# Optimization experiments

Measured on AMD Instinct MI355X. Metric: run time of the kernel, lower is better.

The kernel has to match this reference:

```python
import jax, jax.numpy as jnp
import numpy as np

B, T, HID, H = 4, 2048, 768, 12
D = HID // H  # head_dim = 64


def setup_inputs() -> dict:
    key = jax.random.key(0)
    ks = jax.random.split(key, 8)
    s = 0.02  # keep logits in a sane range
    return {
        "hidden_states": jax.random.normal(ks[0], (B, T, HID), dtype=jnp.float32),
        "attention_mask": jax.random.normal(ks[1], (B, 1, 1, T), dtype=jnp.float32),
        "Wq": jax.random.normal(ks[2], (HID, HID), dtype=jnp.float32) * s,
        "bq": jax.random.normal(ks[3], (HID,), dtype=jnp.float32) * s,
        "Wk": jax.random.normal(ks[4], (HID, HID), dtype=jnp.float32) * s,
        "bk": jax.random.normal(ks[5], (HID,), dtype=jnp.float32) * s,
        "Wv": jax.random.normal(ks[6], (HID, HID), dtype=jnp.float32) * s,
        "bv": jax.random.normal(ks[7], (HID,), dtype=jnp.float32) * s,
    }


def _split_heads(x):
    # [B, T, HID] -> [B, H, T, D]
    b, t, _ = x.shape
    return x.reshape(b, t, H, D).transpose(0, 2, 1, 3)


def reference(hidden_states, attention_mask, Wq, bq, Wk, bk, Wv, bv):
    # nn.Linear: y = x @ W^T + b
    q = _split_heads(hidden_states @ Wq.T + bq)  # [B,H,T,D]
    k = _split_heads(hidden_states @ Wk.T + bk)
    v = _split_heads(hidden_states @ Wv.T + bv)

    scores = jnp.einsum("bhqd,bhkd->bhqk", q, k) / jnp.sqrt(jnp.float32(D))
    causal = jnp.tril(jnp.ones((T, T), dtype=bool))[None, None]  # [1,1,T,T]
    neg_inf = jnp.finfo(scores.dtype).min
    scores = jnp.where(causal, scores, neg_inf)
    # attention_mask here is a float additive mask (randn: min<0, max>1 branch)
    scores = scores + attention_mask

    probs = jax.nn.softmax(scores, axis=-1)  # [B,H,T,T]
    ctx = jnp.einsum("bhqk,bhkd->bhqd", probs, v)  # [B,H,T,D]
    return ctx.transpose(0, 2, 1, 3).reshape(B, T, HID)
```

## Files before the change

### kernel.cpp

```cpp
#include <hip/hip_runtime.h>
#include <hip/hip_bf16.h>
#include <stdint.h>

typedef __attribute__((ext_vector_type(8))) short short8x;
typedef __attribute__((ext_vector_type(4))) float float4x;
typedef __attribute__((ext_vector_type(2))) unsigned int uint2x;

#define B_SZ 4
#define T_SEQ 2048
#define HID_SZ 768
#define NH 12
#define HD 64
#define LDP 72
#define QBLK 64
#define NT 32

__device__ __forceinline__ unsigned short f2b(float f) {
    union { float f; unsigned int u; } v; v.f = f;
    unsigned int u = v.u;
    u += 0x7fffu + ((u >> 16) & 1u);
    return (unsigned short)(u >> 16);
}

__device__ __forceinline__ unsigned int pkbf(float a, float b) {
    __hip_bfloat162 p = __float22bfloat162_rn(make_float2(a, b));
    return *(unsigned int*)&p;
}

__global__ __launch_bounds__(256) void qkv_gemm(
    const float* __restrict__ X,
    const float* __restrict__ Wq, const float* __restrict__ bq,
    const float* __restrict__ Wk, const float* __restrict__ bk,
    const float* __restrict__ Wv, const float* __restrict__ bv,
    unsigned short* __restrict__ Yq, unsigned short* __restrict__ Yk,
    unsigned short* __restrict__ Yv)
{
    const int z = blockIdx.z;
    const float* W    = (z == 0) ? Wq : (z == 1) ? Wk : Wv;
    const float* bias = (z == 0) ? bq : (z == 1) ? bk : bv;
    unsigned short* Y = (z == 0) ? Yq : (z == 1) ? Yk : Yv;

    __shared__ unsigned short As[128 * LDP];
    __shared__ unsigned short Bs[128 * LDP];
    const int tid  = threadIdx.x;
    const int lane = tid & 63;
    const int w    = tid >> 6;
    const int bm = blockIdx.x, bn = blockIdx.y;
    const int wm = (w >> 1) * 64, wn = (w & 1) * 64;
    const int lr = lane & 15;
    const int hi = lane >> 4;

    float4x acc[4][4];
#pragma unroll
    for (int i = 0; i < 4; ++i)
#pragma unroll
        for (int j = 0; j < 4; ++j) acc[i][j] = (float4x)0.0f;

    for (int k0 = 0; k0 < HID_SZ; k0 += 64) {
        __syncthreads();
#pragma unroll
        for (int i = 0; i < 8; ++i) {
            int f4 = tid + i * 256;
            int row = f4 >> 4, c4 = f4 & 15;
            float4 va = *(const float4*)(X + (size_t)(bm * 128 + row) * HID_SZ + k0 + c4 * 4);
            uint2x ua; ua.x = pkbf(va.x, va.y); ua.y = pkbf(va.z, va.w);
            *(uint2x*)&As[row * LDP + c4 * 4] = ua;
            float4 vb = *(const float4*)(W + (size_t)(bn * 128 + row) * HID_SZ + k0 + c4 * 4);
            uint2x ub; ub.x = pkbf(vb.x, vb.y); ub.y = pkbf(vb.z, vb.w);
            *(uint2x*)&Bs[row * LDP + c4 * 4] = ub;
        }
        __syncthreads();

        short8x a[4][2], bf[4][2];
#pragma unroll
        for (int rf = 0; rf < 4; ++rf)
#pragma unroll
            for (int ks = 0; ks < 2; ++ks)
                a[rf][ks] = *(const short8x*)&As[(wm + rf * 16 + lr) * LDP + ks * 32 + hi * 8];
#pragma unroll
        for (int cf = 0; cf < 4; ++cf)
#pragma unroll
            for (int ks = 0; ks < 2; ++ks)
                bf[cf][ks] = *(const short8x*)&Bs[(wn + cf * 16 + lr) * LDP + ks * 32 + hi * 8];
        __builtin_amdgcn_s_setprio(1);
#pragma unroll
        for (int rf = 0; rf < 4; ++rf)
#pragma unroll
            for (int cf = 0; cf < 4; ++cf)
#pragma unroll
                for (int ks = 0; ks < 2; ++ks)
                    acc[rf][cf] = __builtin_amdgcn_mfma_f32_16x16x32_bf16(
                        a[rf][ks], bf[cf][ks], acc[rf][cf], 0, 0, 0);
        __builtin_amdgcn_s_setprio(0);
    }

#pragma unroll
    for (int rf = 0; rf < 4; ++rf)
#pragma unroll
        for (int cf = 0; cf < 4; ++cf) {
            int n = bn * 128 + wn + cf * 16 + lr;
            float bv = bias[n];
            int h = n >> 6, d = n & 63;
#pragma unroll
            for (int reg = 0; reg < 4; ++reg) {
                int m = bm * 128 + wm + rf * 16 + hi * 4 + reg;
                int b = m >> 11, t = m & 2047;
                Y[(((size_t)b * NH + h) * T_SEQ + t) * HD + d] = f2b(acc[rf][cf][reg] + bv);
            }
        }
}

__global__ __launch_bounds__(256) void attn(
    const unsigned short* __restrict__ Q, const unsigned short* __restrict__ K,
    const unsigned short* __restrict__ V, const float* __restrict__ mask,
    float* __restrict__ out)
{
    __shared__ unsigned short Vt[2][HD * LDP];
    __shared__ unsigned short Ps[4][16 * LDP];
    __shared__ float Ms[T_SEQ];

    const int tid = threadIdx.x, lane = tid & 63, w = tid >> 6;
    const int lr = lane & 15, hi = lane >> 4;
    const int bh = blockIdx.x;
    const int jj = NT - 1 - blockIdx.y;
    const int b = bh / NH, h = bh % NH;
    const size_t base = (size_t)bh * T_SEQ * HD;
    const int q0 = jj * QBLK;

    {
        int t8 = tid * 8;
        *(float4*)&Ms[t8]     = *(const float4*)&mask[b * T_SEQ + t8];
        *(float4*)&Ms[t8 + 4] = *(const float4*)&mask[b * T_SEQ + t8 + 4];
    }

    const int c8 = tid & 7;
    const int r0 = tid >> 3;
    const int r1 = r0 + 32;
    const int pr0 = r0 ^ (c8 << 3);
    const int pr1 = r1 ^ (c8 << 3);

    short8x qa[2];
#pragma unroll
    for (int ks = 0; ks < 2; ++ks)
        qa[ks] = *(const short8x*)(Q + base + (size_t)(q0 + w * 16 + lr) * HD + ks * 32 + hi * 8);

    float4x o[4];
    float mrun = -3.0e38f, lrun = 0.0f;
#pragma unroll
    for (int j = 0; j < 4; ++j) o[j] = (float4x)0.0f;

    {
        short8x v0 = *(const short8x*)(V + base + (size_t)r0 * HD + c8 * 8);
        short8x v1 = *(const short8x*)(V + base + (size_t)r1 * HD + c8 * 8);
#pragma unroll
        for (int j = 0; j < 8; ++j) {
            Vt[0][(c8 * 8 + j) * LDP + pr0] = (unsigned short)v0[j];
            Vt[0][(c8 * 8 + j) * LDP + pr1] = (unsigned short)v1[j];
        }
    }
    __syncthreads();

    int cur = 0;
    int kv = 0;
    short8x kb0[4][2], kb1[4][2];
#pragma unroll
    for (int c = 0; c < 4; ++c)
#pragma unroll
        for (int ks = 0; ks < 2; ++ks)
            kb0[c][ks] = *(const short8x*)(K + base + (size_t)(c * 16 + lr) * HD + ks * 32 + hi * 8);

    auto body = [&](short8x (&kb)[4][2], short8x (&kbn)[4][2]) -> bool {
        const bool pf = (kv < jj);
        short8x nv0, nv1;
        if (pf) {
#pragma unroll
            for (int c = 0; c < 4; ++c)
#pragma unroll
                for (int ks = 0; ks < 2; ++ks)
                    kbn[c][ks] = *(const short8x*)(K + base + (size_t)((kv + 1) * 64 + c * 16 + lr) * HD + ks * 32 + hi * 8);
            nv0 = *(const short8x*)(V + base + (size_t)((kv + 1) * 64 + r0) * HD + c8 * 8);
            nv1 = *(const short8x*)(V + base + (size_t)((kv + 1) * 64 + r1) * HD + c8 * 8);
        }

        float4x s[4];
        __builtin_amdgcn_s_setprio(1);
#pragma unroll
        for (int c = 0; c < 4; ++c) {
            s[c] = (float4x)0.0f;
#pragma unroll
            for (int ks = 0; ks < 2; ++ks)
                s[c] = __builtin_amdgcn_mfma_f32_16x16x32_bf16(
                    kb[c][ks], qa[ks], s[c], 0, 0, 0);
        }
        __builtin_amdgcn_s_setprio(0);

        const bool diag = (kv == jj);
        const int qloc = w * 16 + lr;
#pragma unroll
        for (int c = 0; c < 4; ++c) {
            float4 mv = *(const float4*)&Ms[kv * 64 + c * 16 + hi * 4];
#pragma unroll
            for (int reg = 0; reg < 4; ++reg) {
                float x = s[c][reg] * 0.125f + ((const float*)&mv)[reg];
                if (diag) {
                    int kloc = c * 16 + hi * 4 + reg;
                    if (kloc > qloc) x = -1.0e30f;
                }
                s[c][reg] = x;
            }
        }

        float tm = -3.0e38f;
#pragma unroll
        for (int c = 0; c < 4; ++c)
#pragma unroll
            for (int reg = 0; reg < 4; ++reg) tm = fmaxf(tm, s[c][reg]);
        tm = fmaxf(tm, __shfl_xor(tm, 16, 64));
        tm = fmaxf(tm, __shfl_xor(tm, 32, 64));
        float mn = fmaxf(mrun, tm);
        float corr = __expf(mrun - mn);
        mrun = mn;
        float ps = 0.0f;
#pragma unroll
        for (int c = 0; c < 4; ++c)
#pragma unroll
            for (int reg = 0; reg < 4; ++reg) {
                float p = __expf(s[c][reg] - mn);
                s[c][reg] = p;
                ps += p;
            }
        ps += __shfl_xor(ps, 16, 64);
        ps += __shfl_xor(ps, 32, 64);
        lrun = lrun * corr + ps;
#pragma unroll
        for (int cf = 0; cf < 4; ++cf) o[cf] *= corr;

#pragma unroll
        for (int c = 0; c < 4; ++c) {
            uint2x pk;
            pk.x = pkbf(s[c][0], s[c][1]);
            pk.y = pkbf(s[c][2], s[c][3]);
            *(uint2x*)&Ps[w][lr * LDP + c * 16 + hi * 4] = pk;
        }

        short8x pa[2], vb[4][2];
#pragma unroll
        for (int ks = 0; ks < 2; ++ks)
            pa[ks] = *(const short8x*)&Ps[w][lr * LDP + ks * 32 + hi * 8];
#pragma unroll
        for (int cf = 0; cf < 4; ++cf)
#pragma unroll
            for (int ks = 0; ks < 2; ++ks) {
                int d = cf * 16 + lr;
                int pcb = (ks * 32 + hi * 8) ^ (((d >> 3) & 7) << 3);
                vb[cf][ks] = *(const short8x*)&Vt[cur][d * LDP + pcb];
            }
        __builtin_amdgcn_s_setprio(1);
#pragma unroll
        for (int cf = 0; cf < 4; ++cf)
#pragma unroll
            for (int ks = 0; ks < 2; ++ks)
                o[cf] = __builtin_amdgcn_mfma_f32_16x16x32_bf16(
                    vb[cf][ks], pa[ks], o[cf], 0, 0, 0);
        __builtin_amdgcn_s_setprio(0);

        if (pf) {
            int nxt = cur ^ 1;
#pragma unroll
            for (int j = 0; j < 8; ++j) {
                Vt[nxt][(c8 * 8 + j) * LDP + pr0] = (unsigned short)nv0[j];
                Vt[nxt][(c8 * 8 + j) * LDP + pr1] = (unsigned short)nv1[j];
            }
            __syncthreads();
            cur = nxt;
        }
        ++kv;
        return pf;
    };

    while (true) {
        if (!body(kb0, kb1)) break;
        if (!body(kb1, kb0)) break;
    }

    float inv = 1.0f / lrun;
    int t = q0 + w * 16 + lr;
#pragma unroll
    for (int cf = 0; cf < 4; ++cf) {
        float4 st;
        st.x = o[cf][0] * inv; st.y = o[cf][1] * inv;
        st.z = o[cf][2] * inv; st.w = o[cf][3] * inv;
        *(float4*)(out + ((size_t)b * T_SEQ + t) * HID_SZ + h * HD + cf * 16 + hi * 4) = st;
    }
}

extern "C" void kernel_launch(void* const* d_in, const int* in_sizes, int n_in,
                              void* d_out, int out_size, void* d_ws, size_t ws_size,
                              hipStream_t stream) {
    const float* X    = (const float*)d_in[0];
    const float* mask = (const float*)d_in[1];
    const float* Wq   = (const float*)d_in[2];
    const float* bq   = (const float*)d_in[3];
    const float* Wk   = (const float*)d_in[4];
    const float* bk   = (const float*)d_in[5];
    const float* Wv   = (const float*)d_in[6];
    const float* bv   = (const float*)d_in[7];
    float* out = (float*)d_out;

    unsigned short* qw = (unsigned short*)d_ws;
    unsigned short* kw = qw + (size_t)B_SZ * T_SEQ * HID_SZ;
    unsigned short* vw = kw + (size_t)B_SZ * T_SEQ * HID_SZ;

    dim3 blk(256);
    qkv_gemm<<<dim3(64, 6, 3), blk, 0, stream>>>(X, Wq, bq, Wk, bk, Wv, bv, qw, kw, vw);
    attn<<<dim3(48, NT), blk, 0, stream>>>(qw, kw, vw, mask, out);
}
```

Baseline: 178.7 us.

## Use exp2 softmax with lazy max rescaling and deferred row-sum reduction

Result: no change. 178.3 us (-0.2%).

```diff
diff --git a/kernel.cpp b/kernel.cpp
--- a/kernel.cpp
+++ b/kernel.cpp
@@ -14,6 +14,9 @@
 #define LDP 72
 #define QBLK 64
 #define NT 32
+#define LOG2E 1.4426950408889634f
+#define SCL2 0.18033688011112043f
+#define DTHR 8.0f
 
 __device__ __forceinline__ unsigned short f2b(float f) {
     union { float f; unsigned int u; } v; v.f = f;
@@ -129,8 +132,12 @@
 
     {
         int t8 = tid * 8;
-        *(float4*)&Ms[t8]     = *(const float4*)&mask[b * T_SEQ + t8];
-        *(float4*)&Ms[t8 + 4] = *(const float4*)&mask[b * T_SEQ + t8 + 4];
+        float4 m0 = *(const float4*)&mask[b * T_SEQ + t8];
+        float4 m1 = *(const float4*)&mask[b * T_SEQ + t8 + 4];
+        m0.x *= LOG2E; m0.y *= LOG2E; m0.z *= LOG2E; m0.w *= LOG2E;
+        m1.x *= LOG2E; m1.y *= LOG2E; m1.z *= LOG2E; m1.w *= LOG2E;
+        *(float4*)&Ms[t8]     = m0;
+        *(float4*)&Ms[t8 + 4] = m1;
     }
 
     const int c8 = tid & 7;
@@ -145,7 +152,7 @@
         qa[ks] = *(const short8x*)(Q + base + (size_t)(q0 + w * 16 + lr) * HD + ks * 32 + hi * 8);
 
     float4x o[4];
-    float mrun = -3.0e38f, lrun = 0.0f;
+    float mrun = -3.0e38f, lp = 0.0f;
 #pragma unroll
     for (int j = 0; j < 4; ++j) o[j] = (float4x)0.0f;
 
@@ -201,7 +208,7 @@
             float4 mv = *(const float4*)&Ms[kv * 64 + c * 16 + hi * 4];
 #pragma unroll
             for (int reg = 0; reg < 4; ++reg) {
-                float x = s[c][reg] * 0.125f + ((const float*)&mv)[reg];
+                float x = s[c][reg] * SCL2 + ((const float*)&mv)[reg];
                 if (diag) {
                     int kloc = c * 16 + hi * 4 + reg;
                     if (kloc > qloc) x = -1.0e30f;
@@ -210,30 +217,31 @@
             }
         }
 
-        float tm = -3.0e38f;
+        float ptm = -3.0e38f;
 #pragma unroll
         for (int c = 0; c < 4; ++c)
 #pragma unroll
-            for (int reg = 0; reg < 4; ++reg) tm = fmaxf(tm, s[c][reg]);
-        tm = fmaxf(tm, __shfl_xor(tm, 16, 64));
-        tm = fmaxf(tm, __shfl_xor(tm, 32, 64));
-        float mn = fmaxf(mrun, tm);
-        float corr = __expf(mrun - mn);
-        mrun = mn;
+            for (int reg = 0; reg < 4; ++reg) ptm = fmaxf(ptm, s[c][reg]);
+        if (!__all(ptm <= mrun + DTHR)) {
+            float tm = fmaxf(ptm, __shfl_xor(ptm, 16, 64));
+            tm = fmaxf(tm, __shfl_xor(tm, 32, 64));
+            float mn = fmaxf(mrun, tm);
+            float corr = exp2f(mrun - mn);
+            mrun = mn;
+            lp *= corr;
+#pragma unroll
+            for (int cf = 0; cf < 4; ++cf) o[cf] *= corr;
+        }
         float ps = 0.0f;
 #pragma unroll
         for (int c = 0; c < 4; ++c)
 #pragma unroll
             for (int reg = 0; reg < 4; ++reg) {
-                float p = __expf(s[c][reg] - mn);
+                float p = exp2f(s[c][reg] - mrun);
                 s[c][reg] = p;
                 ps += p;
             }
-        ps += __shfl_xor(ps, 16, 64);
-        ps += __shfl_xor(ps, 32, 64);
-        lrun = lrun * corr + ps;
-#pragma unroll
-        for (int cf = 0; cf < 4; ++cf) o[cf] *= corr;
+        lp += ps;
 
 #pragma unroll
         for (int c = 0; c < 4; ++c) {
@@ -283,7 +291,11 @@
         if (!body(kb1, kb0)) break;
     }
 
-    float inv = 1.0f / lrun;
+    float lsum = lp;
+    lsum += __shfl_xor(lsum, 16, 64);
+    lsum += __shfl_xor(lsum, 32, 64);
+    float inv = 1.0f / lsum;
+
     int t = q0 + w * 16 + lr;
 #pragma unroll
     for (int cf = 0; cf < 4; ++cf) {
```
